# Kernel tuning notes

Measured on AMD Instinct MI355X. Metric: run time of the kernel, lower is better.

## Reference

```python
import jax, jax.numpy as jnp
import numpy as np

B, T, E = 64, 1024, 128          # batch, max_len, embedding_size
C, F = 5, 64                     # context_len, convolutional_filters
H = C // 2                       # half-window


def setup_inputs() -> dict:
    key = jax.random.key(0)
    k1, k2 = jax.random.split(key)
    x = jax.random.normal(k1, (B, T, E), dtype=jnp.float32)
    # Conv2d(1, F, (E*C, 1)) weight, flattened: W[f, k] with k = c*E + e
    # (context windows are concatenated embedding vectors, disc = -H..H)
    W = jax.random.normal(k2, (F, C * E), dtype=jnp.float32) * 0.05
    b = jnp.zeros((F,), dtype=jnp.float32)
    return {"x": x, "W": W, "b": b}


def reference(x, W, b):
    # sentence_to_Z_vector: zero-pad H positions on each side, then for each
    # position t concatenate embeddings of t-H .. t+H  -> [B, T, C*E]
    Bx, Tx, Ex = x.shape
    xp = jnp.pad(x, ((0, 0), (H, H), (0, 0)))
    # stack C shifted views (C is a small constant, loop is over kernel taps)
    Z = jnp.stack([xp[:, i:i + Tx] for i in range(C)], axis=2)  # [B, T, C, E]
    Z = Z.reshape(Bx, Tx, C * Ex)                               # [B, T, C*E]
    # degenerate full-height Conv2d == per-position matmul -> [B, F, T]
    out = jnp.einsum('btk,fk->bft', Z, W) + b[None, :, None]
    return out
```

## Files before the change

### kernel.cpp

```cpp
#include <hip/hip_runtime.h>
#include <stdint.h>

#define Bdim 64
#define Tdim 1024
#define Edim 128
#define Cdim 5
#define Fdim 64
#define Hpad 2

#define TTILE 128
#define XROWS (TTILE + Cdim - 1)
#define LDSTR (Edim + 8)

typedef __attribute__((ext_vector_type(8))) short short8;
typedef __attribute__((ext_vector_type(4))) float float4v;
typedef __attribute__((ext_vector_type(4))) unsigned short ushort4v;

__device__ __forceinline__ unsigned short f2bf(float f) {
    union { float f; uint32_t u; } v; v.f = f;
    uint32_t u = v.u;
    u += 0x7fffu + ((u >> 16) & 1u);
    return (unsigned short)(u >> 16);
}

__global__ __launch_bounds__(256, 2)
void qa_cnn_kernel(const float* __restrict__ x, const float* __restrict__ W,
                   const float* __restrict__ bias, float* __restrict__ out) {
    __shared__ __align__(16) unsigned short sX[XROWS * LDSTR];
    __shared__ __align__(16) unsigned short sW[Fdim * LDSTR];

    const int tid = threadIdx.x;
    const int tt  = blockIdx.x;
    const int b   = blockIdx.y;
    const int t0  = tt * TTILE;

    {
        const int nslots = XROWS * (Edim / 4);
        for (int idx = tid; idx < nslots; idx += 256) {
            const int row = idx >> 5;
            const int c4  = idx & 31;
            const int gt  = t0 - Hpad + row;
            float4v v = {0.f, 0.f, 0.f, 0.f};
            if (gt >= 0 && gt < Tdim) {
                v = *(const float4v*)(x + ((size_t)b * Tdim + gt) * Edim + c4 * 4);
            }
            ushort4v o = { f2bf(v.x), f2bf(v.y), f2bf(v.z), f2bf(v.w) };
            *(ushort4v*)&sX[row * LDSTR + c4 * 4] = o;
        }
    }

    const int wave = tid >> 6;
    const int lane = tid & 63;
    const int m16  = lane & 15;
    const int quad = lane >> 4;

    float4v acc[2][4];
    #pragma unroll
    for (int i = 0; i < 2; ++i)
        #pragma unroll
        for (int j = 0; j < 4; ++j) acc[i][j] = (float4v){0.f, 0.f, 0.f, 0.f};

    for (int c = 0; c < Cdim; ++c) {
        __syncthreads();
        for (int idx = tid; idx < Fdim * (Edim / 4); idx += 256) {
            const int f  = idx >> 5;
            const int c4 = idx & 31;
            float4v v = *(const float4v*)(W + (size_t)f * (Cdim * Edim) + c * Edim + c4 * 4);
            ushort4v o = { f2bf(v.x), f2bf(v.y), f2bf(v.z), f2bf(v.w) };
            *(ushort4v*)&sW[f * LDSTR + c4 * 4] = o;
        }
        __syncthreads();

        #pragma unroll
        for (int kk = 0; kk < Edim; kk += 32) {
            const int kcol = kk + quad * 8;
            short8 afrag[2];
            #pragma unroll
            for (int mt = 0; mt < 2; ++mt) {
                const int row = c + wave * 32 + mt * 16 + m16;
                afrag[mt] = *(const short8*)&sX[row * LDSTR + kcol];
            }
            #pragma unroll
            for (int nt = 0; nt < 4; ++nt) {
                const short8 bfrag = *(const short8*)&sW[(nt * 16 + m16) * LDSTR + kcol];
                #pragma unroll
                for (int mt = 0; mt < 2; ++mt) {
                    acc[mt][nt] = __builtin_amdgcn_mfma_f32_16x16x32_bf16(
                        afrag[mt], bfrag, acc[mt][nt], 0, 0, 0);
                }
            }
        }
    }

    #pragma unroll
    for (int nt = 0; nt < 4; ++nt) {
        const int f  = nt * 16 + m16;
        const float bv = bias[f];
        #pragma unroll
        for (int mt = 0; mt < 2; ++mt) {
            const int t = t0 + wave * 32 + mt * 16 + quad * 4;
            float4v v = acc[mt][nt];
            v.x += bv; v.y += bv; v.z += bv; v.w += bv;
            *(float4v*)(out + ((size_t)b * Fdim + f) * Tdim + t) = v;
        }
    }
}

extern "C" void kernel_launch(void* const* d_in, const int* in_sizes, int n_in,
                              void* d_out, int out_size, void* d_ws, size_t ws_size,
                              hipStream_t stream) {
    const float* x    = (const float*)d_in[0];
    const float* W    = (const float*)d_in[1];
    const float* bias = (const float*)d_in[2];
    float* out = (float*)d_out;

    dim3 grid(Tdim / TTILE, Bdim);
    dim3 block(256);
    qa_cnn_kernel<<<grid, block, 0, stream>>>(x, W, bias, out);
}
```

Measured before the change: 97.37 us.

## Pre-convert W to bf16 once and load B fragments directly from global

Adds a separate kernel that converts W to bf16 in the workspace each call. The main kernel then drops the shared-memory W staging and the per-tap barriers, and reads B fragments straight from global/L2 into registers. The work is also remapped so each wave owns 16 filters across all 64 time positions, with the tile halved to 64 and occupancy raised to 4 blocks per SM. The cost is an extra launch and more, smaller blocks that each reload the x halo rows.

```diff
diff --git a/kernel.cpp b/kernel.cpp
--- a/kernel.cpp
+++ b/kernel.cpp
@@ -7,8 +7,9 @@
 #define Cdim 5
 #define Fdim 64
 #define Hpad 2
+#define Kdim (Cdim * Edim)
 
-#define TTILE 128
+#define TTILE 64
 #define XROWS (TTILE + Cdim - 1)
 #define LDSTR (Edim + 8)
 
@@ -23,11 +24,19 @@
     return (unsigned short)(u >> 16);
 }
 
-__global__ __launch_bounds__(256, 2)
-void qa_cnn_kernel(const float* __restrict__ x, const float* __restrict__ W,
-                   const float* __restrict__ bias, float* __restrict__ out) {
+__global__ void convert_W(const float* __restrict__ W, unsigned short* __restrict__ Wbf) {
+    int i = blockIdx.x * 256 + threadIdx.x;
+    if (i < (Fdim * Kdim) / 4) {
+        float4v v = ((const float4v*)W)[i];
+        ushort4v o = { f2bf(v.x), f2bf(v.y), f2bf(v.z), f2bf(v.w) };
+        ((ushort4v*)Wbf)[i] = o;
+    }
+}
+
+__global__ __launch_bounds__(256, 4)
+void qa_cnn_main(const float* __restrict__ x, const unsigned short* __restrict__ Wbf,
+                 const float* __restrict__ bias, float* __restrict__ out) {
     __shared__ __align__(16) unsigned short sX[XROWS * LDSTR];
-    __shared__ __align__(16) unsigned short sW[Fdim * LDSTR];
 
     const int tid = threadIdx.x;
     const int tt  = blockIdx.x;
@@ -48,61 +57,45 @@
             *(ushort4v*)&sX[row * LDSTR + c4 * 4] = o;
         }
     }
+    __syncthreads();
 
     const int wave = tid >> 6;
     const int lane = tid & 63;
     const int m16  = lane & 15;
     const int quad = lane >> 4;
 
-    float4v acc[2][4];
+    const unsigned short* wrow = Wbf + (size_t)(wave * 16 + m16) * Kdim + quad * 8;
+
+    float4v acc[4];
     #pragma unroll
-    for (int i = 0; i < 2; ++i)
+    for (int mt = 0; mt < 4; ++mt) acc[mt] = (float4v){0.f, 0.f, 0.f, 0.f};
+
+    #pragma unroll
+    for (int c = 0; c < Cdim; ++c) {
+        short8 bfrag[4];
         #pragma unroll
-        for (int j = 0; j < 4; ++j) acc[i][j] = (float4v){0.f, 0.f, 0.f, 0.f};
-
-    for (int c = 0; c < Cdim; ++c) {
-        __syncthreads();
-        for (int idx = tid; idx < Fdim * (Edim / 4); idx += 256) {
-            const int f  = idx >> 5;
-            const int c4 = idx & 31;
-            float4v v = *(const float4v*)(W + (size_t)f * (Cdim * Edim) + c * Edim + c4 * 4);
-            ushort4v o = { f2bf(v.x), f2bf(v.y), f2bf(v.z), f2bf(v.w) };
-            *(ushort4v*)&sW[f * LDSTR + c4 * 4] = o;
-        }
-        __syncthreads();
+        for (int kk = 0; kk < 4; ++kk)
+            bfrag[kk] = *(const short8*)(wrow + c * Edim + kk * 32);
 
         #pragma unroll
-        for (int kk = 0; kk < Edim; kk += 32) {
-            const int kcol = kk + quad * 8;
-            short8 afrag[2];
+        for (int kk = 0; kk < 4; ++kk) {
+            const int kcol = kk * 32 + quad * 8;
             #pragma unroll
-            for (int mt = 0; mt < 2; ++mt) {
-                const int row = c + wave * 32 + mt * 16 + m16;
-                afrag[mt] = *(const short8*)&sX[row * LDSTR + kcol];
-            }
-            #pragma unroll
-            for (int nt = 0; nt < 4; ++nt) {
-                const short8 bfrag = *(const short8*)&sW[(nt * 16 + m16) * LDSTR + kcol];
-                #pragma unroll
-                for (int mt = 0; mt < 2; ++mt) {
-                    acc[mt][nt] = __builtin_amdgcn_mfma_f32_16x16x32_bf16(
-                        afrag[mt], bfrag, acc[mt][nt], 0, 0, 0);
-                }
+            for (int mt = 0; mt < 4; ++mt) {
+                const short8 a = *(const short8*)&sX[(c + mt * 16 + m16) * LDSTR + kcol];
+                acc[mt] = __builtin_amdgcn_mfma_f32_16x16x32_bf16(a, bfrag[kk], acc[mt], 0, 0, 0);
             }
         }
     }
 
+    const int f  = wave * 16 + m16;
+    const float bv = bias[f];
+    float* orow = out + ((size_t)b * Fdim + f) * Tdim + t0 + quad * 4;
     #pragma unroll
-    for (int nt = 0; nt < 4; ++nt) {
-        const int f  = nt * 16 + m16;
-        const float bv = bias[f];
-        #pragma unroll
-        for (int mt = 0; mt < 2; ++mt) {
-            const int t = t0 + wave * 32 + mt * 16 + quad * 4;
-            float4v v = acc[mt][nt];
-            v.x += bv; v.y += bv; v.z += bv; v.w += bv;
-            *(float4v*)(out + ((size_t)b * Fdim + f) * Tdim + t) = v;
-        }
+    for (int mt = 0; mt < 4; ++mt) {
+        float4v v = acc[mt];
+        v.x += bv; v.y += bv; v.z += bv; v.w += bv;
+        *(float4v*)(orow + mt * 16) = v;
     }
 }
 
@@ -113,8 +106,8 @@
     const float* W    = (const float*)d_in[1];
     const float* bias = (const float*)d_in[2];
     float* out = (float*)d_out;
+    unsigned short* Wbf = (unsigned short*)d_ws;
 
-    dim3 grid(Tdim / TTILE, Bdim);
-    dim3 block(256);
-    qa_cnn_kernel<<<grid, block, 0, stream>>>(x, W, bias, out);
+    convert_W<<<dim3((Fdim * Kdim / 4 + 255) / 256), dim3(256), 0, stream>>>(W, Wbf);
+    qa_cnn_main<<<dim3(Tdim / TTILE, Bdim), dim3(256), 0, stream>>>(x, Wbf, bias, out);
 }
```

Measured after the change: 92.34 us. 5.2% less time.
